# Kernel tuning notes

Measured on AMD Instinct MI355X. Metric: run time of the kernel, lower is better.

Reference implementation:

```python
import jax, jax.numpy as jnp
import numpy as np

DEPTH = 7  # complete binary trees with 2**DEPTH = 128 leaves

B, L = 4096, 128
V, E, OUT = 100000, 128, 3


def setup_inputs() -> dict:
    key = jax.random.key(0)
    ks = jax.random.split(key, 6)
    tokens = jax.random.randint(ks[0], (B, L), 0, V, dtype=jnp.int64)
    embedding = jax.random.normal(ks[1], (V, E), dtype=jnp.float32)
    # tree_layer: Linear(2E -> E); torch stores weight as [out, in]
    W_tree = jax.random.normal(ks[2], (E, 2 * E), dtype=jnp.float32) * (1.0 / np.sqrt(2 * E))
    b_tree = jax.random.normal(ks[3], (E,), dtype=jnp.float32) * 0.01
    # classifier_layer: Linear(E -> OUT)
    W_cls = jax.random.normal(ks[4], (OUT, E), dtype=jnp.float32) * (1.0 / np.sqrt(E))
    b_cls = jax.random.normal(ks[5], (OUT,), dtype=jnp.float32) * 0.01
    return {"tokens": tokens, "embedding": embedding, "W_tree": W_tree,
            "b_tree": b_tree, "W_cls": W_cls, "b_cls": b_cls}


def reference(tokens, embedding, W_tree, b_tree, W_cls, b_cls):
    # Leaf embeddings: gather rows of the embedding table. [B, L, E]
    reps = embedding[tokens]
    # Level-synchronous bottom-up composition (depth-batched across all trees):
    # at each level, pair adjacent nodes, concat features, apply tree_layer + tanh.
    for _ in range(DEPTH):
        left = reps[:, 0::2, :]   # [B, n/2, E]
        right = reps[:, 1::2, :]  # [B, n/2, E]
        combined = jnp.concatenate([left, right], axis=-1)  # [B, n/2, 2E]
        reps = jnp.tanh(jnp.einsum('bnh,eh->bne', combined, W_tree) + b_tree)
    roots = reps[:, 0, :]  # [B, E]
    return roots @ W_cls.T + b_cls  # [B, OUT]
```

## Files before the change

kernel.cpp:

```cpp
#include <hip/hip_runtime.h>
#include <hip/hip_fp16.h>


typedef _Float16 half8 __attribute__((ext_vector_type(8)));
typedef float floatx4 __attribute__((ext_vector_type(4)));

#define STRIDE 264
#define UROW   33
#define NPAIR  2048

__device__ __forceinline__ void bar() {
  asm volatile("s_waitcnt lgkmcnt(0)" ::: "memory");
  __builtin_amdgcn_sched_barrier(0);
  __builtin_amdgcn_s_barrier();
  __builtin_amdgcn_sched_barrier(0);
}

__device__ __forceinline__ float fast_tanh(float x) {
  float e = __expf(2.f * x);
  return 1.f - 2.f * __builtin_amdgcn_rcpf(e + 1.f);
}

__device__ __forceinline__ unsigned pkrtz(float a, float b) {
  auto h = __builtin_amdgcn_cvt_pkrtz(a, b);
  return __builtin_bit_cast(unsigned, h);
}

__device__ __forceinline__ void load8(const float* __restrict__ emb, int tok, int seg,
                                      int h, float4 (&x)[8]) {
  const float4* src = (const float4*)emb + (size_t)tok * 32 + (seg & 1) * 16 + 8 * h;
#pragma unroll
  for (int j = 0; j < 8; ++j) x[j] = src[j];
}

__device__ __forceinline__ void gather_cvt_write(const float4 (&x)[8], _Float16* buf,
                                                 int row, int seg, int h) {
  uint4* dst = (uint4*)buf + row * UROW + seg * 8 + 4 * h;
#pragma unroll
  for (int j = 0; j < 4; ++j) {
    float4 a = x[2 * j], b = x[2 * j + 1];
    uint4 w;
    w.x = pkrtz(a.x, a.y); w.y = pkrtz(a.z, a.w);
    w.z = pkrtz(b.x, b.y); w.w = pkrtz(b.z, b.w);
    dst[j] = w;
  }
}

__device__ __forceinline__ void mfma_k256(const _Float16* arow, const half8 (&Wf)[2][8],
                                          const float (&bias)[2], floatx4 (&accO)[2]) {
  floatx4 aA[2], aB[2];
#pragma unroll
  for (int i = 0; i < 2; ++i) {
    aA[i] = (floatx4){bias[i], bias[i], bias[i], bias[i]};
    aB[i] = (floatx4){0.f, 0.f, 0.f, 0.f};
  }
#pragma unroll
  for (int ks = 0; ks < 4; ++ks) {
    half8 x0 = *(const half8*)(arow + ks * 32);
    half8 x1 = *(const half8*)(arow + (ks + 4) * 32);
    aA[0] = __builtin_amdgcn_mfma_f32_16x16x32_f16(x0, Wf[0][ks],     aA[0], 0, 0, 0);
    aB[0] = __builtin_amdgcn_mfma_f32_16x16x32_f16(x1, Wf[0][ks + 4], aB[0], 0, 0, 0);
    aA[1] = __builtin_amdgcn_mfma_f32_16x16x32_f16(x0, Wf[1][ks],     aA[1], 0, 0, 0);
    aB[1] = __builtin_amdgcn_mfma_f32_16x16x32_f16(x1, Wf[1][ks + 4], aB[1], 0, 0, 0);
  }
  accO[0] = aA[0] + aB[0];
  accO[1] = aA[1] + aB[1];
}

template<int MT, int MOUT>
__device__ __forceinline__ void level_std(
    const _Float16* inb, _Float16* outb,
    const half8 (&Wf)[2][8], const float (&bias)[2],
    int nbase, int l15, int quad)
{
  floatx4 acc[MT][2];
#pragma unroll
  for (int m = 0; m < MT; ++m) {
    floatx4 a2[2];
    mfma_k256(inb + (m * 16 + l15) * STRIDE + quad * 8, Wf, bias, a2);
    acc[m][0] = a2[0]; acc[m][1] = a2[1];
  }

  const int mrow = quad * 4;
#pragma unroll
  for (int m = 0; m < MT; ++m)
#pragma unroll
    for (int i = 0; i < 2; ++i) {
      const int col = (nbase + i) * 16 + l15;
#pragma unroll
      for (int r = 0; r < 4; ++r) {
        const int node = m * 16 + mrow + r;
        if (node < MOUT) {
          float v = fast_tanh(acc[m][i][r]);
          outb[(node >> 1) * STRIDE + (node & 1) * 128 + col] = (_Float16)v;
        }
      }
    }
}

__global__ __launch_bounds__(256, 3)
void tree_kernel(const int* __restrict__ tokens,
                 const float* __restrict__ embedding,
                 const float* __restrict__ W_tree,
                 const float* __restrict__ b_tree,
                 const float* __restrict__ W_cls,
                 const float* __restrict__ b_cls,
                 float* __restrict__ out)
{
  __shared__ __align__(16) _Float16 bufA[64 * STRIDE];
  __shared__ __align__(16) _Float16 bufB[32 * STRIDE];
  __shared__ __align__(16) _Float16 bufC[4 * STRIDE];
  __shared__ float wavepart[4][2][3];

  const int tid  = threadIdx.x;
  const int wid  = tid >> 6;
  const int lane = tid & 63;
  const int l15  = lane & 15;
  const int quad = lane >> 4;
  const int nbase = wid * 2;
  const int row  = tid & 63;
  const int seg  = tid >> 6;
  const int tidx = 2 * row + (seg >> 1);

  half8 Wf[2][8];
#pragma unroll
  for (int i = 0; i < 2; ++i) {
    const int e = (nbase + i) * 16 + l15;
#pragma unroll
    for (int ks = 0; ks < 8; ++ks) {
      const int k = ks * 32 + quad * 8;
      const float4* p = (const float4*)(W_tree + e * 256 + k);
      float4 lo = p[0], hi = p[1];
      half8 f;
      f[0] = (_Float16)lo.x; f[1] = (_Float16)lo.y; f[2] = (_Float16)lo.z; f[3] = (_Float16)lo.w;
      f[4] = (_Float16)hi.x; f[5] = (_Float16)hi.y; f[6] = (_Float16)hi.z; f[7] = (_Float16)hi.w;
      Wf[i][ks] = f;
    }
  }
  float bias[2];
#pragma unroll
  for (int i = 0; i < 2; ++i) bias[i] = b_tree[(nbase + i) * 16 + l15];

  float wc[2][3];
#pragma unroll
  for (int i = 0; i < 2; ++i) {
    const int col = (nbase + i) * 16 + l15;
#pragma unroll
    for (int o = 0; o < 3; ++o) wc[i][o] = W_cls[o * 128 + col];
  }

  int tokA = tokens[(2 * blockIdx.x) * 128 + tidx];
  int tokB = tokens[(2 * blockIdx.x + 1) * 128 + tidx];
  float4 pfA[8];
  load8(embedding, tokA, seg, 0, pfA);

#pragma unroll 1
  for (int p = blockIdx.x; p < NPAIR; p += gridDim.x) {
    int pn = p + gridDim.x;
    if (pn >= NPAIR) pn = p;

    float4 x1[8];
    load8(embedding, tokA, seg, 1, x1);
    const int tokAn = tokens[(2 * pn) * 128 + tidx];
    const int tokBn = tokens[(2 * pn + 1) * 128 + tidx];
    gather_cvt_write(pfA, bufA, row, seg, 0);
    gather_cvt_write(x1,  bufA, row, seg, 1);
    bar();

    level_std<4, 64>(bufA, bufB, Wf, bias, nbase, l15, quad);
    float4 pfB[8];
    load8(embedding, tokB, seg, 0, pfB);
    bar();
    level_std<2, 32>(bufB, bufA, Wf, bias, nbase, l15, quad);
    bar();
    level_std<1, 16>(bufA, bufB, Wf, bias, nbase, l15, quad);
    bar();
    level_std<1,  8>(bufB, bufA, Wf, bias, nbase, l15, quad);
    bar();
    level_std<1,  4>(bufA, bufC, Wf, bias, nbase, l15, quad);
    bar();

    load8(embedding, tokB, seg, 1, x1);
    gather_cvt_write(pfB, bufA, row, seg, 0);
    gather_cvt_write(x1,  bufA, row, seg, 1);
    bar();

    level_std<4, 64>(bufA, bufB, Wf, bias, nbase, l15, quad);
    load8(embedding, tokAn, seg, 0, pfA);
    bar();
    level_std<2, 32>(bufB, bufA, Wf, bias, nbase, l15, quad);
    bar();
    level_std<1, 16>(bufA, bufB, Wf, bias, nbase, l15, quad);
    bar();
    level_std<1,  8>(bufB, bufA, Wf, bias, nbase, l15, quad);
    bar();
    level_std<1,  4>(bufA, bufC + 2 * STRIDE, Wf, bias, nbase, l15, quad);
    bar();

    {
      const int rclamp = l15 < 4 ? l15 : 3;
      floatx4 acc[2];
      mfma_k256(bufC + rclamp * STRIDE + quad * 8, Wf, bias, acc);
      const int mrow = quad * 4;
#pragma unroll
      for (int i = 0; i < 2; ++i) {
        const int col = (nbase + i) * 16 + l15;
#pragma unroll
        for (int r = 0; r < 4; ++r) {
          const int mr = mrow + r;
          if (mr < 4) {
            float v = fast_tanh(acc[i][r]);
            bufA[(mr >> 1) * STRIDE + (mr & 1) * 128 + col] = (_Float16)v;
          }
        }
      }
    }
    bar();

    {
      floatx4 acc[2];
      mfma_k256(bufA + l15 * STRIDE + quad * 8, Wf, bias, acc);
      float part[2][3] = {{0.f, 0.f, 0.f}, {0.f, 0.f, 0.f}};
      if (quad == 0) {
#pragma unroll
        for (int i = 0; i < 2; ++i) {
#pragma unroll
          for (int rr = 0; rr < 2; ++rr) {
            float v = fast_tanh(acc[i][rr]);
#pragma unroll
            for (int o = 0; o < 3; ++o) part[rr][o] = fmaf(v, wc[i][o], part[rr][o]);
          }
        }
      }
#pragma unroll
      for (int rr = 0; rr < 2; ++rr) {
#pragma unroll
        for (int o = 0; o < 3; ++o) {
          float v = part[rr][o];
          v += __shfl_down(v, 8);
          v += __shfl_down(v, 4);
          v += __shfl_down(v, 2);
          v += __shfl_down(v, 1);
          if (lane == 0) wavepart[wid][rr][o] = v;
        }
      }
    }
    bar();
    if (tid < 6) {
      const int rr = tid / 3, o = tid - 3 * rr;
      float v = wavepart[0][rr][o] + wavepart[1][rr][o]
              + wavepart[2][rr][o] + wavepart[3][rr][o];
      out[(2 * p + rr) * 3 + o] = v + b_cls[o];
    }
    tokA = tokAn; tokB = tokBn;
  }
}

extern "C" void kernel_launch(void* const* d_in, const int* in_sizes, int n_in,
                              void* d_out, int out_size, void* d_ws, size_t ws_size,
                              hipStream_t stream) {
  const int*   tokens    = (const int*)d_in[0];
  const float* embedding = (const float*)d_in[1];
  const float* W_tree    = (const float*)d_in[2];
  const float* b_tree    = (const float*)d_in[3];
  const float* W_cls     = (const float*)d_in[4];
  const float* b_cls     = (const float*)d_in[5];
  float* out = (float*)d_out;

  dim3 grid(768), block(256);
  tree_kernel<<<grid, block, 0, stream>>>(tokens, embedding, W_tree, b_tree, W_cls, b_cls, out);
}
```

Baseline: 157.6 us.

## Use 8 waves per block with one output tile each, drop register prefetch

Doubles the block to 512 threads so each wave owns a single 16-column output tile, which halves the per-wave weight registers and MFMA work per level. The embedding gather is split into quarters across 8 waves and written straight to LDS. The register-held software prefetch of the next tree's embeddings is removed. This trades gather/compute overlap for more waves per CU and more parallelism within a block, at the cost of more barrier participants.

New measurement: 186.6 us. 18.4% more time.

```diff
diff --git a/kernel.cpp b/kernel.cpp
--- a/kernel.cpp
+++ b/kernel.cpp
@@ -26,16 +26,13 @@
   return __builtin_bit_cast(unsigned, h);
 }
 
-__device__ __forceinline__ void load8(const float* __restrict__ emb, int tok, int seg,
-                                      int h, float4 (&x)[8]) {
-  const float4* src = (const float4*)emb + (size_t)tok * 32 + (seg & 1) * 16 + 8 * h;
+__device__ __forceinline__ void gather_quarter(int tok, const float* __restrict__ emb,
+                                               _Float16* buf, int row, int lb, int q) {
+  const float4* src = (const float4*)emb + (size_t)tok * 32 + q * 8;
+  uint4* dst = (uint4*)buf + row * UROW + lb * 16 + q * 4;
+  float4 x[8];
 #pragma unroll
   for (int j = 0; j < 8; ++j) x[j] = src[j];
-}
-
-__device__ __forceinline__ void gather_cvt_write(const float4 (&x)[8], _Float16* buf,
-                                                 int row, int seg, int h) {
-  uint4* dst = (uint4*)buf + row * UROW + seg * 8 + 4 * h;
 #pragma unroll
   for (int j = 0; j < 4; ++j) {
     float4 a = x[2 * j], b = x[2 * j + 1];
@@ -46,59 +43,44 @@
   }
 }
 
-__device__ __forceinline__ void mfma_k256(const _Float16* arow, const half8 (&Wf)[2][8],
-                                          const float (&bias)[2], floatx4 (&accO)[2]) {
-  floatx4 aA[2], aB[2];
-#pragma unroll
-  for (int i = 0; i < 2; ++i) {
-    aA[i] = (floatx4){bias[i], bias[i], bias[i], bias[i]};
-    aB[i] = (floatx4){0.f, 0.f, 0.f, 0.f};
-  }
+__device__ __forceinline__ floatx4 mfma_k256(const _Float16* arow, const half8 (&Wf)[8],
+                                             float bias) {
+  floatx4 aA = (floatx4){bias, bias, bias, bias};
+  floatx4 aB = (floatx4){0.f, 0.f, 0.f, 0.f};
 #pragma unroll
   for (int ks = 0; ks < 4; ++ks) {
     half8 x0 = *(const half8*)(arow + ks * 32);
     half8 x1 = *(const half8*)(arow + (ks + 4) * 32);
-    aA[0] = __builtin_amdgcn_mfma_f32_16x16x32_f16(x0, Wf[0][ks],     aA[0], 0, 0, 0);
-    aB[0] = __builtin_amdgcn_mfma_f32_16x16x32_f16(x1, Wf[0][ks + 4], aB[0], 0, 0, 0);
-    aA[1] = __builtin_amdgcn_mfma_f32_16x16x32_f16(x0, Wf[1][ks],     aA[1], 0, 0, 0);
-    aB[1] = __builtin_amdgcn_mfma_f32_16x16x32_f16(x1, Wf[1][ks + 4], aB[1], 0, 0, 0);
-  }
-  accO[0] = aA[0] + aB[0];
-  accO[1] = aA[1] + aB[1];
+    aA = __builtin_amdgcn_mfma_f32_16x16x32_f16(x0, Wf[ks],     aA, 0, 0, 0);
+    aB = __builtin_amdgcn_mfma_f32_16x16x32_f16(x1, Wf[ks + 4], aB, 0, 0, 0);
+  }
+  return aA + aB;
 }
 
 template<int MT, int MOUT>
 __device__ __forceinline__ void level_std(
     const _Float16* inb, _Float16* outb,
-    const half8 (&Wf)[2][8], const float (&bias)[2],
-    int nbase, int l15, int quad)
+    const half8 (&Wf)[8], float bias, int col, int l15, int quad)
 {
-  floatx4 acc[MT][2];
-#pragma unroll
-  for (int m = 0; m < MT; ++m) {
-    floatx4 a2[2];
-    mfma_k256(inb + (m * 16 + l15) * STRIDE + quad * 8, Wf, bias, a2);
-    acc[m][0] = a2[0]; acc[m][1] = a2[1];
-  }
+  floatx4 acc[MT];
+#pragma unroll
+  for (int m = 0; m < MT; ++m)
+    acc[m] = mfma_k256(inb + (m * 16 + l15) * STRIDE + quad * 8, Wf, bias);
 
   const int mrow = quad * 4;
 #pragma unroll
   for (int m = 0; m < MT; ++m)
 #pragma unroll
-    for (int i = 0; i < 2; ++i) {
-      const int col = (nbase + i) * 16 + l15;
-#pragma unroll
-      for (int r = 0; r < 4; ++r) {
-        const int node = m * 16 + mrow + r;
-        if (node < MOUT) {
-          float v = fast_tanh(acc[m][i][r]);
-          outb[(node >> 1) * STRIDE + (node & 1) * 128 + col] = (_Float16)v;
-        }
-      }
-    }
-}
-
-__global__ __launch_bounds__(256, 3)
+    for (int r = 0; r < 4; ++r) {
+      const int node = m * 16 + mrow + r;
+      if (node < MOUT) {
+        float v = fast_tanh(acc[m][r]);
+        outb[(node >> 1) * STRIDE + (node & 1) * 128 + col] = (_Float16)v;
+      }
+    }
+}
+
+__global__ __launch_bounds__(512, 6)
 void tree_kernel(const int* __restrict__ tokens,
                  const float* __restrict__ embedding,
                  const float* __restrict__ W_tree,
@@ -110,126 +92,99 @@
   __shared__ __align__(16) _Float16 bufA[64 * STRIDE];
   __shared__ __align__(16) _Float16 bufB[32 * STRIDE];
   __shared__ __align__(16) _Float16 bufC[4 * STRIDE];
-  __shared__ float wavepart[4][2][3];
+  __shared__ float wavepart[8][2][3];
 
   const int tid  = threadIdx.x;
   const int wid  = tid >> 6;
   const int lane = tid & 63;
   const int l15  = lane & 15;
   const int quad = lane >> 4;
-  const int nbase = wid * 2;
+  const int col  = wid * 16 + l15;
   const int row  = tid & 63;
   const int seg  = tid >> 6;
-  const int tidx = 2 * row + (seg >> 1);
-
-  half8 Wf[2][8];
-#pragma unroll
-  for (int i = 0; i < 2; ++i) {
-    const int e = (nbase + i) * 16 + l15;
-#pragma unroll
-    for (int ks = 0; ks < 8; ++ks) {
-      const int k = ks * 32 + quad * 8;
-      const float4* p = (const float4*)(W_tree + e * 256 + k);
-      float4 lo = p[0], hi = p[1];
-      half8 f;
-      f[0] = (_Float16)lo.x; f[1] = (_Float16)lo.y; f[2] = (_Float16)lo.z; f[3] = (_Float16)lo.w;
-      f[4] = (_Float16)hi.x; f[5] = (_Float16)hi.y; f[6] = (_Float16)hi.z; f[7] = (_Float16)hi.w;
-      Wf[i][ks] = f;
-    }
-  }
-  float bias[2];
-#pragma unroll
-  for (int i = 0; i < 2; ++i) bias[i] = b_tree[(nbase + i) * 16 + l15];
-
-  float wc[2][3];
-#pragma unroll
-  for (int i = 0; i < 2; ++i) {
-    const int col = (nbase + i) * 16 + l15;
-#pragma unroll
-    for (int o = 0; o < 3; ++o) wc[i][o] = W_cls[o * 128 + col];
-  }
+  const int lb   = seg >> 2;
+  const int q    = seg & 3;
+  const int tidx = 2 * row + lb;
+
+  half8 Wf[8];
+#pragma unroll
+  for (int ks = 0; ks < 8; ++ks) {
+    const int k = ks * 32 + quad * 8;
+    const float4* p = (const float4*)(W_tree + col * 256 + k);
+    float4 lo = p[0], hi = p[1];
+    half8 f;
+    f[0] = (_Float16)lo.x; f[1] = (_Float16)lo.y; f[2] = (_Float16)lo.z; f[3] = (_Float16)lo.w;
+    f[4] = (_Float16)hi.x; f[5] = (_Float16)hi.y; f[6] = (_Float16)hi.z; f[7] = (_Float16)hi.w;
+    Wf[ks] = f;
+  }
+  const float bias = b_tree[col];
+
+  float wc[3];
+#pragma unroll
+  for (int o = 0; o < 3; ++o) wc[o] = W_cls[o * 128 + col];
 
   int tokA = tokens[(2 * blockIdx.x) * 128 + tidx];
   int tokB = tokens[(2 * blockIdx.x + 1) * 128 + tidx];
-  float4 pfA[8];
-  load8(embedding, tokA, seg, 0, pfA);
 
 #pragma unroll 1
   for (int p = blockIdx.x; p < NPAIR; p += gridDim.x) {
     int pn = p + gridDim.x;
     if (pn >= NPAIR) pn = p;
 
-    float4 x1[8];
-    load8(embedding, tokA, seg, 1, x1);
+    gather_quarter(tokA, embedding, bufA, row, lb, q);
     const int tokAn = tokens[(2 * pn) * 128 + tidx];
     const int tokBn = tokens[(2 * pn + 1) * 128 + tidx];
-    gather_cvt_write(pfA, bufA, row, seg, 0);
-    gather_cvt_write(x1,  bufA, row, seg, 1);
-    bar();
-
-    level_std<4, 64>(bufA, bufB, Wf, bias, nbase, l15, quad);
-    float4 pfB[8];
-    load8(embedding, tokB, seg, 0, pfB);
-    bar();
-    level_std<2, 32>(bufB, bufA, Wf, bias, nbase, l15, quad);
-    bar();
-    level_std<1, 16>(bufA, bufB, Wf, bias, nbase, l15, quad);
-    bar();
-    level_std<1,  8>(bufB, bufA, Wf, bias, nbase, l15, quad);
-    bar();
-    level_std<1,  4>(bufA, bufC, Wf, bias, nbase, l15, quad);
-    bar();
-
-    load8(embedding, tokB, seg, 1, x1);
-    gather_cvt_write(pfB, bufA, row, seg, 0);
-    gather_cvt_write(x1,  bufA, row, seg, 1);
-    bar();
-
-    level_std<4, 64>(bufA, bufB, Wf, bias, nbase, l15, quad);
-    load8(embedding, tokAn, seg, 0, pfA);
-    bar();
-    level_std<2, 32>(bufB, bufA, Wf, bias, nbase, l15, quad);
-    bar();
-    level_std<1, 16>(bufA, bufB, Wf, bias, nbase, l15, quad);
-    bar();
-    level_std<1,  8>(bufB, bufA, Wf, bias, nbase, l15, quad);
-    bar();
-    level_std<1,  4>(bufA, bufC + 2 * STRIDE, Wf, bias, nbase, l15, quad);
+    bar();
+
+    level_std<4, 64>(bufA, bufB, Wf, bias, col, l15, quad);
+    bar();
+    level_std<2, 32>(bufB, bufA, Wf, bias, col, l15, quad);
+    bar();
+    level_std<1, 16>(bufA, bufB, Wf, bias, col, l15, quad);
+    bar();
+    level_std<1,  8>(bufB, bufA, Wf, bias, col, l15, quad);
+    bar();
+    level_std<1,  4>(bufA, bufC, Wf, bias, col, l15, quad);
+    bar();
+
+    gather_quarter(tokB, embedding, bufA, row, lb, q);
+    bar();
+
+    level_std<4, 64>(bufA, bufB, Wf, bias, col, l15, quad);
+    bar();
+    level_std<2, 32>(bufB, bufA, Wf, bias, col, l15, quad);
+    bar();
+    level_std<1, 16>(bufA, bufB, Wf, bias, col, l15, quad);
+    bar();
+    level_std<1,  8>(bufB, bufA, Wf, bias, col, l15, quad);
+    bar();
+    level_std<1,  4>(bufA, bufC + 2 * STRIDE, Wf, bias, col, l15, quad);
     bar();
 
     {
       const int rclamp = l15 < 4 ? l15 : 3;
-      floatx4 acc[2];
-      mfma_k256(bufC + rclamp * STRIDE + quad * 8, Wf, bias, acc);
+      floatx4 acc = mfma_k256(bufC + rclamp * STRIDE + quad * 8, Wf, bias);
       const int mrow = quad * 4;
 #pragma unroll
-      for (int i = 0; i < 2; ++i) {
-        const int col = (nbase + i) * 16 + l15;
-#pragma unroll
-        for (int r = 0; r < 4; ++r) {
-          const int mr = mrow + r;
-          if (mr < 4) {
-            float v = fast_tanh(acc[i][r]);
-            bufA[(mr >> 1) * STRIDE + (mr & 1) * 128 + col] = (_Float16)v;
-          }
+      for (int r = 0; r < 4; ++r) {
+        const int mr = mrow + r;
+        if (mr < 4) {
+          float v = fast_tanh(acc[r]);
+          bufA[(mr >> 1) * STRIDE + (mr & 1) * 128 + col] = (_Float16)v;
         }
       }
     }
     bar();
 
     {
-      floatx4 acc[2];
-      mfma_k256(bufA + l15 * STRIDE + quad * 8, Wf, bias, acc);
+      floatx4 acc = mfma_k256(bufA + l15 * STRIDE + quad * 8, Wf, bias);
       float part[2][3] = {{0.f, 0.f, 0.f}, {0.f, 0.f, 0.f}};
       if (quad == 0) {
 #pragma unroll
-        for (int i = 0; i < 2; ++i) {
-#pragma unroll
-          for (int rr = 0; rr < 2; ++rr) {
-            float v = fast_tanh(acc[i][rr]);
-#pragma unroll
-            for (int o = 0; o < 3; ++o) part[rr][o] = fmaf(v, wc[i][o], part[rr][o]);
-          }
+        for (int rr = 0; rr < 2; ++rr) {
+          float v = fast_tanh(acc[rr]);
+#pragma unroll
+          for (int o = 0; o < 3; ++o) part[rr][o] = fmaf(v, wc[o], part[rr][o]);
         }
       }
 #pragma unroll
@@ -248,8 +203,9 @@
     bar();
     if (tid < 6) {
       const int rr = tid / 3, o = tid - 3 * rr;
-      float v = wavepart[0][rr][o] + wavepart[1][rr][o]
-              + wavepart[2][rr][o] + wavepart[3][rr][o];
+      float v = 0.f;
+#pragma unroll
+      for (int w = 0; w < 8; ++w) v += wavepart[w][rr][o];
       out[(2 * p + rr) * 3 + o] = v + b_cls[o];
     }
     tokA = tokAn; tokB = tokBn;
@@ -267,6 +223,6 @@
   const float* b_cls     = (const float*)d_in[5];
   float* out = (float*)d_out;
 
-  dim3 grid(768), block(256);
+  dim3 grid(768), block(512);
   tree_kernel<<<grid, block, 0, stream>>>(tokens, embedding, W_tree, b_tree, W_cls, b_cls, out);
 }
```
